# Kernel optimization log

Hardware: AMD Instinct MI355X
Metric: run time of the kernel (lower is better)

Reference implementation:

```python
import jax, jax.numpy as jnp
import numpy as np

N = 100000  # nodes
K = 6       # kNN neighbors (includes self, loop=True)


def _knn_edges(pos_np, k):
    """Exact kNN with self-loops, chunked to bound memory. Returns (src, dst) int32."""
    n = pos_np.shape[0]
    idx = np.empty((n, k), dtype=np.int32)
    sq = (pos_np ** 2).sum(1)
    cs = 512
    for s in range(0, n, cs):
        e = min(s + cs, n)
        d = sq[s:e, None] - 2.0 * (pos_np[s:e] @ pos_np.T) + sq[None, :]
        idx[s:e] = np.argpartition(d, k, axis=1)[:, :k].astype(np.int32)
    src = idx.reshape(-1)                                  # neighbors j
    dst = np.repeat(np.arange(n, dtype=np.int32), k)       # centers i
    return src, dst


def _linear_init(key, fan_in, fan_out):
    k1, k2 = jax.random.split(key)
    s = 1.0 / np.sqrt(fan_in)
    W = jax.random.uniform(k1, (fan_in, fan_out), minval=-s, maxval=s, dtype=jnp.float32)
    b = jax.random.uniform(k2, (fan_out,), minval=-s, maxval=s, dtype=jnp.float32)
    return W, b


def setup_inputs() -> dict:
    rng = np.random.default_rng(0)
    pos_np = rng.standard_normal((N, 3)).astype(np.float32)
    src, dst = _knn_edges(pos_np, K)
    edge_index = jnp.asarray(np.stack([src, dst]))

    key = jax.random.key(0)
    ks = jax.random.split(key, 6)
    W1a, b1a = _linear_init(ks[0], 3 + 3, 32)
    W1b, b1b = _linear_init(ks[1], 32, 32)
    W2a, b2a = _linear_init(ks[2], 32 + 3, 64)
    W2b, b2b = _linear_init(ks[3], 64, 64)
    W3a, b3a = _linear_init(ks[4], 64 + 3, 128)
    W3b, b3b = _linear_init(ks[5], 128, 128)

    return dict(pos=jnp.asarray(pos_np), edge_index=edge_index,
                W1a=W1a, b1a=b1a, W1b=W1b, b1b=b1b,
                W2a=W2a, b2a=b2a, W2b=W2b, b2b=b2b,
                W3a=W3a, b3a=b3a, W3b=W3b, b3b=b3b)


def _pointnet_conv(x, pos, src, dst, Wa, ba, Wb, bb):
    # message per edge (j->i): local_nn(concat(x_j, pos_j - pos_i)); max-aggregate at i
    m = jnp.concatenate([x[src], pos[src] - pos[dst]], axis=-1)  # [E, Cin+3]
    m = jax.nn.relu(m @ Wa + ba) @ Wb + bb                       # [E, Cout]
    return jax.ops.segment_max(m, dst, num_segments=N)           # [N, Cout]


def reference(pos, edge_index, W1a, b1a, W1b, b1b, W2a, b2a, W2b, b2b, W3a, b3a, W3b, b3b):
    src, dst = edge_index[0], edge_index[1]
    h = jax.nn.relu(_pointnet_conv(pos, pos, src, dst, W1a, b1a, W1b, b1b))
    h = jax.nn.relu(_pointnet_conv(h, pos, src, dst, W2a, b2a, W2b, b2b))
    h = jax.nn.relu(_pointnet_conv(h, pos, src, dst, W3a, b3a, W3b, b3b))
    return h
```

## Files before the change

### kernel.cpp

```cpp
#include <hip/hip_runtime.h>

#define NODES 100000
#define KNN 6

typedef unsigned short u16t;
typedef __attribute__((ext_vector_type(8))) short bf16x8;
typedef __attribute__((ext_vector_type(4))) float f32x4;
union U16 { uint4 u; bf16x8 b; };

__device__ inline f32x4 mfma16(bf16x8 a, bf16x8 b, f32x4 c) {
    return __builtin_amdgcn_mfma_f32_16x16x32_bf16(a, b, c, 0, 0, 0);
}
__device__ inline unsigned top2(unsigned u1, unsigned u0) {
    return __builtin_amdgcn_perm(u1, u0, 0x07060302u);
}
__device__ inline u16t bf16_rn(float x) {
    unsigned u = __float_as_uint(x);
    return (u16t)((u + 0x7FFF + ((u >> 16) & 1)) >> 16);
}
__device__ inline float bf16_f(u16t h) {
    return __uint_as_float(((unsigned)h) << 16);
}
__device__ inline void split_store(u16t* hp, u16t* lp, float v) {
    const unsigned u = __float_as_uint(v);
    *hp = (u16t)(u >> 16);
    const float hif = __uint_as_float(u & 0xFFFF0000u);
    *lp = (u16t)(__float_as_uint(v - hif) >> 16);
}

template <int CIN_, int N_>
__device__ void prep_dev(const float* __restrict__ W,
                         uint4* __restrict__ fh, uint4* __restrict__ fl, int idx) {
    constexpr int KT = (CIN_ + 31) / 32;
    constexpr int NTt = N_ / 16;
    if (idx >= NTt * KT * 64) return;
    const int lane = idx & 63;
    const int fk = idx >> 6;
    const int kt = fk % KT, t = fk / KT;
    const int n = t * 16 + (lane & 15);
    const int kbase = kt * 32 + (lane >> 4) * 8;
    unsigned h[4], l[4];
    for (int p = 0; p < 4; p++) {
        u16t hh[2], ll[2];
        for (int q = 0; q < 2; q++) {
            const int c = kbase + 2 * p + q;
            const float w = (c < CIN_) ? W[(size_t)c * N_ + n] : 0.f;
            const u16t hi = bf16_rn(w);
            hh[q] = hi;
            ll[q] = bf16_rn(w - bf16_f(hi));
        }
        h[p] = (unsigned)hh[0] | ((unsigned)hh[1] << 16);
        l[p] = (unsigned)ll[0] | ((unsigned)ll[1] << 16);
    }
    fh[idx] = make_uint4(h[0], h[1], h[2], h[3]);
    fl[idx] = make_uint4(l[0], l[1], l[2], l[3]);
}

__global__ void prep_all(const float* W1a, const float* W1b,
                         const float* W2a, const float* W2b,
                         const float* W3a, const float* W3b, uint4* wf) {
    const int b = blockIdx.x, t = threadIdx.x;
    if (b == 0)      prep_dev<6, 32>(W1a, wf + 0, wf + 128, t);
    else if (b == 1) prep_dev<32, 32>(W1b, wf + 256, wf + 384, t);
    else if (b < 4)  prep_dev<35, 64>(W2a, wf + 512, wf + 1024, (b - 2) * 256 + t);
    else if (b < 6)  prep_dev<64, 64>(W2b, wf + 1536, wf + 2048, (b - 4) * 256 + t);
    else if (b < 12) prep_dev<67, 128>(W3a, wf + 2560, wf + 4096, (b - 6) * 256 + t);
    else             prep_dev<128, 128>(W3b, wf + 5632, wf + 7680, (b - 12) * 256 + t);
}

template <int CX, int H, int NWAVE, int NB, bool OUTP>
__global__ __launch_bounds__(NWAVE * 64, 4) void pnconv_mfma(
    const u16t* __restrict__ xh, const u16t* __restrict__ xl,
    const float* __restrict__ pos, const int* __restrict__ ei,
    const uint4* __restrict__ wfa_hi, const uint4* __restrict__ wfa_lo,
    const float* __restrict__ ba,
    const uint4* __restrict__ wfb_hi, const uint4* __restrict__ wfb_lo,
    const float* __restrict__ bb,
    float* __restrict__ outf, u16t* __restrict__ oh, u16t* __restrict__ ol)
{
    constexpr int NTH = NWAVE * 64;
    constexpr int CIN = CX + 3;
    constexpr int K1T = (CIN + 31) / 32;
    constexpr int K2T = H / 32;
    constexpr int NW = (H / 16) / NWAVE;
    constexpr int E = NB * KNN;
    constexpr int MT1 = E / 16;
    constexpr int MT2 = E / 16;
    constexpr int K1P = K1T * 32 + 8;
    constexpr int K2P = K2T * 32 + 8;
    constexpr int APL = E * K1P;
    constexpr int HPL = E * K2P;
    constexpr int SM = (2 * APL > 2 * HPL) ? 2 * APL : 2 * HPL;
    static_assert(E % 48 == 0 && E <= NTH, "tile shape");
    static_assert(MT2 % 3 == 0, "slot perm needs m-triples");

    __shared__ __align__(16) u16t smem[SM];
    __shared__ int srcs[E];

    const int tid = threadIdx.x;
    const int lane = tid & 63, wv = tid >> 6;
    const int l15 = lane & 15, quad = lane >> 4;
    const int node0 = blockIdx.x * NB;
    const long e0 = (long)node0 * KNN;

    if (tid < E) srcs[tid] = ei[e0 + tid];

    U16 wah[2][NW], wal[2][NW];
#pragma unroll
    for (int t = 0; t < NW; t++) {
        const int fi = ((wv * NW + t) * K1T) * 64 + lane;
        wah[0][t].u = wfa_hi[fi];
        wal[0][t].u = wfa_lo[fi];
    }
    __syncthreads();

    if constexpr (CX % 8 == 0) {
        constexpr int C8 = CX / 8;
        for (int i = tid; i < E * C8; i += NTH) {
            const int e = i / C8, c0 = i % C8;
            const int c = (c0 + e) & (C8 - 1);
            const size_t sb = (size_t)srcs[e] * CX + c * 8;
            *(uint4*)&smem[e * K1P + c * 8] = *(const uint4*)&xh[sb];
            *(uint4*)&smem[APL + e * K1P + c * 8] = *(const uint4*)&xl[sb];
        }
    }
    for (int i = tid; i < E * 3; i += NTH) {
        const int e = i / 3, d = i - 3 * (i / 3);
        const int s = srcs[e], nd = node0 + e / KNN;
        const float sp = pos[3 * s + d];
        if constexpr (CX == 3)
            split_store(&smem[e * K1P + d], &smem[APL + e * K1P + d], sp);
        split_store(&smem[e * K1P + CX + d], &smem[APL + e * K1P + CX + d],
                    sp - pos[3 * nd + d]);
    }
    constexpr int PADA = (CIN + 7) & ~7;
    constexpr int NU4 = (K1P - PADA) / 8;
    for (int i = tid; i < 2 * E; i += NTH) {
        const int pl = (i >= E) ? 1 : 0;
        const int e = i - pl * E;
        u16t* row = &smem[pl * APL + e * K1P];
        for (int k = CIN; k < PADA; k++) row[k] = 0;
        for (int j = 0; j < NU4; j++) *(uint4*)&row[PADA + j * 8] = make_uint4(0, 0, 0, 0);
    }
    __syncthreads();

    f32x4 acc1[NW][MT1];
#pragma unroll
    for (int t = 0; t < NW; t++)
#pragma unroll
        for (int m = 0; m < MT1; m++) acc1[t][m] = (f32x4){0.f, 0.f, 0.f, 0.f};

#pragma unroll
    for (int kt = 0; kt < K1T; kt++) {
        const int cur = kt & 1, nxt = cur ^ 1;
        const int nkt = (kt + 1 < K1T) ? kt + 1 : kt;
#pragma unroll
        for (int t = 0; t < NW; t++) {
            const int fi = ((wv * NW + t) * K1T + nkt) * 64 + lane;
            wah[nxt][t].u = wfa_hi[fi];
            wal[nxt][t].u = wfa_lo[fi];
        }
#pragma unroll
        for (int m = 0; m < MT1; m++) {
            const u16t* p = &smem[(m * 16 + l15) * K1P + kt * 32 + quad * 8];
            U16 dh, dl;
            dh.u = *(const uint4*)p;
            dl.u = *(const uint4*)(p + APL);
#pragma unroll
            for (int t = 0; t < NW; t++) {
                acc1[t][m] = mfma16(wah[cur][t].b, dh.b, acc1[t][m]);
                acc1[t][m] = mfma16(wah[cur][t].b, dl.b, acc1[t][m]);
                acc1[t][m] = mfma16(wal[cur][t].b, dh.b, acc1[t][m]);
            }
        }
    }

    U16 wbh[2][NW], wbl[2][NW];
#pragma unroll
    for (int t = 0; t < NW; t++) {
        const int fi = ((wv * NW + t) * K2T) * 64 + lane;
        wbh[0][t].u = wfb_hi[fi];
        wbl[0][t].u = wfb_lo[fi];
    }
    __syncthreads();

#pragma unroll
    for (int t = 0; t < NW; t++) {
        const int khb = (wv * NW + t) * 16 + quad * 4;
        const float4 bs = *(const float4*)&ba[khb];
#pragma unroll
        for (int m = 0; m < MT1; m++) {
            const float v0 = fmaxf(acc1[t][m][0] + bs.x, 0.f);
            const float v1 = fmaxf(acc1[t][m][1] + bs.y, 0.f);
            const float v2 = fmaxf(acc1[t][m][2] + bs.z, 0.f);
            const float v3 = fmaxf(acc1[t][m][3] + bs.w, 0.f);
            const unsigned u0 = __float_as_uint(v0), u1 = __float_as_uint(v1);
            const unsigned u2 = __float_as_uint(v2), u3 = __float_as_uint(v3);
            uint2 hw, lw;
            hw.x = top2(u1, u0);
            hw.y = top2(u3, u2);
            const float l0 = v0 - __uint_as_float(u0 & 0xFFFF0000u);
            const float l1 = v1 - __uint_as_float(u1 & 0xFFFF0000u);
            const float l2 = v2 - __uint_as_float(u2 & 0xFFFF0000u);
            const float l3 = v3 - __uint_as_float(u3 & 0xFFFF0000u);
            lw.x = top2(__float_as_uint(l1), __float_as_uint(l0));
            lw.y = top2(__float_as_uint(l3), __float_as_uint(l2));
            u16t* wp = &smem[(m * 16 + l15) * K2P + khb];
            *(uint2*)wp = hw;
            *(uint2*)(wp + HPL) = lw;
        }
    }
    __syncthreads();

    int eaddr[MT2];
#pragma unroll
    for (int m = 0; m < MT2; m++) {
        const int nd_s = (m / 3) * 8 + 2 * (l15 >> 2) + ((l15 >> 1) & 1);
        const int i_s = (m % 3) * 2 + (l15 & 1);
        eaddr[m] = (nd_s * KNN + i_s) * K2P + quad * 8;
    }

    f32x4 acc2[NW][MT2];
#pragma unroll
    for (int t = 0; t < NW; t++)
#pragma unroll
        for (int m = 0; m < MT2; m++) acc2[t][m] = (f32x4){0.f, 0.f, 0.f, 0.f};

#pragma unroll
    for (int kt = 0; kt < K2T; kt++) {
        const int cur = kt & 1, nxt = cur ^ 1;
        const int nkt = (kt + 1 < K2T) ? kt + 1 : kt;
#pragma unroll
        for (int t = 0; t < NW; t++) {
            const int fi = ((wv * NW + t) * K2T + nkt) * 64 + lane;
            wbh[nxt][t].u = wfb_hi[fi];
            wbl[nxt][t].u = wfb_lo[fi];
        }
#pragma unroll
        for (int m = 0; m < MT2; m++) {
            const u16t* p = &smem[eaddr[m] + kt * 32];
            U16 dh, dl;
            dh.u = *(const uint4*)p;
            dl.u = *(const uint4*)(p + HPL);
#pragma unroll
            for (int t = 0; t < NW; t++) {
                acc2[t][m] = mfma16(dh.b, wbh[cur][t].b, acc2[t][m]);
                acc2[t][m] = mfma16(dh.b, wbl[cur][t].b, acc2[t][m]);
                acc2[t][m] = mfma16(dl.b, wbh[cur][t].b, acc2[t][m]);
            }
        }
    }

#pragma unroll
    for (int t = 0; t < NW; t++) {
        const int nb = (wv * NW + t) * 16;
        const float bias = bb[nb + l15];
#pragma unroll
        for (int g = 0; g < MT2 / 3; g++) {
#pragma unroll
            for (int rp = 0; rp < 2; rp++) {
                float v = fmaxf(
                    fmaxf(fmaxf(acc2[t][3 * g + 0][2 * rp], acc2[t][3 * g + 0][2 * rp + 1]),
                          fmaxf(acc2[t][3 * g + 1][2 * rp], acc2[t][3 * g + 1][2 * rp + 1])),
                    fmaxf(acc2[t][3 * g + 2][2 * rp], acc2[t][3 * g + 2][2 * rp + 1]));
                v = fmaxf(v + bias, 0.f);
                const int node = node0 + g * 8 + 2 * quad + rp;
                const size_t oidx = (size_t)node * H + nb + l15;
                if constexpr (OUTP) {
                    split_store(&oh[oidx], &ol[oidx], v);
                } else {
                    outf[oidx] = v;
                }
            }
        }
    }
}

extern "C" void kernel_launch(void* const* d_in, const int* in_sizes, int n_in,
                              void* d_out, int out_size, void* d_ws, size_t ws_size,
                              hipStream_t stream) {
    const float* pos = (const float*)d_in[0];
    const int* ei = (const int*)d_in[1];
    const float* W1a = (const float*)d_in[2];
    const float* b1a = (const float*)d_in[3];
    const float* W1b = (const float*)d_in[4];
    const float* b1b = (const float*)d_in[5];
    const float* W2a = (const float*)d_in[6];
    const float* b2a = (const float*)d_in[7];
    const float* W2b = (const float*)d_in[8];
    const float* b2b = (const float*)d_in[9];
    const float* W3a = (const float*)d_in[10];
    const float* b3a = (const float*)d_in[11];
    const float* W3b = (const float*)d_in[12];
    const float* b3b = (const float*)d_in[13];

    u16t* h1h = (u16t*)d_ws;
    u16t* h1l = h1h + (size_t)NODES * 32;
    u16t* h2h = h1l + (size_t)NODES * 32;
    u16t* h2l = h2h + (size_t)NODES * 64;
    uint4* wf = (uint4*)(h2l + (size_t)NODES * 64);

    prep_all<<<20, 256, 0, stream>>>(W1a, W1b, W2a, W2b, W3a, W3b, wf);

    pnconv_mfma<3, 32, 2, 16, true><<<NODES / 16, 128, 0, stream>>>(
        nullptr, nullptr, pos, ei,
        wf + 0, wf + 128, b1a, wf + 256, wf + 384, b1b,
        nullptr, h1h, h1l);

    pnconv_mfma<32, 64, 4, 16, true><<<NODES / 16, 256, 0, stream>>>(
        h1h, h1l, pos, ei,
        wf + 512, wf + 1024, b2a, wf + 1536, wf + 2048, b2b,
        nullptr, h2h, h2l);

    pnconv_mfma<64, 128, 4, 8, false><<<NODES / 8, 256, 0, stream>>>(
        h2h, h2l, pos, ei,
        wf + 2560, wf + 4096, b3a, wf + 5632, wf + 7680, b3b,
        (float*)d_out, nullptr, nullptr);
}
```

Measured before the change: 233.0 us.

## Load edge indices into registers and preload all weight fragments upfront

```diff
diff --git a/kernel.cpp b/kernel.cpp
--- a/kernel.cpp
+++ b/kernel.cpp
@@ -27,6 +27,7 @@
     const float hif = __uint_as_float(u & 0xFFFF0000u);
     *lp = (u16t)(__float_as_uint(v - hif) >> 16);
 }
+constexpr int cdiv(int a, int b) { return (a + b - 1) / b; }
 
 template <int CIN_, int N_>
 __device__ void prep_dev(const float* __restrict__ W,
@@ -69,7 +70,7 @@
 }
 
 template <int CX, int H, int NWAVE, int NB, bool OUTP>
-__global__ __launch_bounds__(NWAVE * 64, 4) void pnconv_mfma(
+__device__ __forceinline__ void pnconv_body(
     const u16t* __restrict__ xh, const u16t* __restrict__ xl,
     const float* __restrict__ pos, const int* __restrict__ ei,
     const uint4* __restrict__ wfa_hi, const uint4* __restrict__ wfa_lo,
@@ -91,11 +92,10 @@
     constexpr int APL = E * K1P;
     constexpr int HPL = E * K2P;
     constexpr int SM = (2 * APL > 2 * HPL) ? 2 * APL : 2 * HPL;
-    static_assert(E % 48 == 0 && E <= NTH, "tile shape");
+    static_assert(E % 48 == 0, "tile shape");
     static_assert(MT2 % 3 == 0, "slot perm needs m-triples");
 
     __shared__ __align__(16) u16t smem[SM];
-    __shared__ int srcs[E];
 
     const int tid = threadIdx.x;
     const int lane = tid & 63, wv = tid >> 6;
@@ -103,35 +103,58 @@
     const int node0 = blockIdx.x * NB;
     const long e0 = (long)node0 * KNN;
 
-    if (tid < E) srcs[tid] = ei[e0 + tid];
-
-    U16 wah[2][NW], wal[2][NW];
-#pragma unroll
-    for (int t = 0; t < NW; t++) {
-        const int fi = ((wv * NW + t) * K1T) * 64 + lane;
-        wah[0][t].u = wfa_hi[fi];
-        wal[0][t].u = wfa_lo[fi];
-    }
-    __syncthreads();
-
+    constexpr int C8 = (CX % 8 == 0) ? CX / 8 : 1;
+    constexpr int NGX = (CX % 8 == 0) ? cdiv(E * C8, NTH) : 1;
+    constexpr int NGP = cdiv(E * 3, NTH);
+    int sx_[NGX], sp_[NGP];
     if constexpr (CX % 8 == 0) {
-        constexpr int C8 = CX / 8;
-        for (int i = tid; i < E * C8; i += NTH) {
-            const int e = i / C8, c0 = i % C8;
-            const int c = (c0 + e) & (C8 - 1);
-            const size_t sb = (size_t)srcs[e] * CX + c * 8;
-            *(uint4*)&smem[e * K1P + c * 8] = *(const uint4*)&xh[sb];
-            *(uint4*)&smem[APL + e * K1P + c * 8] = *(const uint4*)&xl[sb];
-        }
-    }
-    for (int i = tid; i < E * 3; i += NTH) {
-        const int e = i / 3, d = i - 3 * (i / 3);
-        const int s = srcs[e], nd = node0 + e / KNN;
-        const float sp = pos[3 * s + d];
-        if constexpr (CX == 3)
-            split_store(&smem[e * K1P + d], &smem[APL + e * K1P + d], sp);
-        split_store(&smem[e * K1P + CX + d], &smem[APL + e * K1P + CX + d],
-                    sp - pos[3 * nd + d]);
+#pragma unroll
+        for (int k = 0; k < NGX; k++) {
+            const int i = tid + k * NTH;
+            sx_[k] = ei[e0 + ((i < E * C8) ? i / C8 : 0)];
+        }
+    }
+#pragma unroll
+    for (int k = 0; k < NGP; k++) {
+        const int i = tid + k * NTH;
+        sp_[k] = ei[e0 + ((i < E * 3) ? i / 3 : 0)];
+    }
+
+    U16 wah[NW][K1T], wal[NW][K1T];
+#pragma unroll
+    for (int t = 0; t < NW; t++)
+#pragma unroll
+        for (int kt = 0; kt < K1T; kt++) {
+            const int fi = ((wv * NW + t) * K1T + kt) * 64 + lane;
+            wah[t][kt].u = wfa_hi[fi];
+            wal[t][kt].u = wfa_lo[fi];
+        }
+
+    if constexpr (CX % 8 == 0) {
+#pragma unroll
+        for (int k = 0; k < NGX; k++) {
+            const int i = tid + k * NTH;
+            if (i < E * C8) {
+                const int e = i / C8, c0 = i % C8;
+                const int c = (c0 + e) & (C8 - 1);
+                const size_t sb = (size_t)sx_[k] * CX + c * 8;
+                *(uint4*)&smem[e * K1P + c * 8] = *(const uint4*)&xh[sb];
+                *(uint4*)&smem[APL + e * K1P + c * 8] = *(const uint4*)&xl[sb];
+            }
+        }
+    }
+#pragma unroll
+    for (int k = 0; k < NGP; k++) {
+        const int i = tid + k * NTH;
+        if (i < E * 3) {
+            const int e = i / 3, d = i - 3 * (i / 3);
+            const int s = sp_[k], nd = node0 + e / KNN;
+            const float sp = pos[3 * s + d];
+            if constexpr (CX == 3)
+                split_store(&smem[e * K1P + d], &smem[APL + e * K1P + d], sp);
+            split_store(&smem[e * K1P + CX + d], &smem[APL + e * K1P + CX + d],
+                        sp - pos[3 * nd + d]);
+        }
     }
     constexpr int PADA = (CIN + 7) & ~7;
     constexpr int NU4 = (K1P - PADA) / 8;
@@ -152,14 +175,6 @@
 
 #pragma unroll
     for (int kt = 0; kt < K1T; kt++) {
-        const int cur = kt & 1, nxt = cur ^ 1;
-        const int nkt = (kt + 1 < K1T) ? kt + 1 : kt;
-#pragma unroll
-        for (int t = 0; t < NW; t++) {
-            const int fi = ((wv * NW + t) * K1T + nkt) * 64 + lane;
-            wah[nxt][t].u = wfa_hi[fi];
-            wal[nxt][t].u = wfa_lo[fi];
-        }
 #pragma unroll
         for (int m = 0; m < MT1; m++) {
             const u16t* p = &smem[(m * 16 + l15) * K1P + kt * 32 + quad * 8];
@@ -168,20 +183,22 @@
             dl.u = *(const uint4*)(p + APL);
 #pragma unroll
             for (int t = 0; t < NW; t++) {
-                acc1[t][m] = mfma16(wah[cur][t].b, dh.b, acc1[t][m]);
-                acc1[t][m] = mfma16(wah[cur][t].b, dl.b, acc1[t][m]);
-                acc1[t][m] = mfma16(wal[cur][t].b, dh.b, acc1[t][m]);
+                acc1[t][m] = mfma16(wah[t][kt].b, dh.b, acc1[t][m]);
+                acc1[t][m] = mfma16(wah[t][kt].b, dl.b, acc1[t][m]);
+                acc1[t][m] = mfma16(wal[t][kt].b, dh.b, acc1[t][m]);
             }
         }
     }
 
-    U16 wbh[2][NW], wbl[2][NW];
-#pragma unroll
-    for (int t = 0; t < NW; t++) {
-        const int fi = ((wv * NW + t) * K2T) * 64 + lane;
-        wbh[0][t].u = wfb_hi[fi];
-        wbl[0][t].u = wfb_lo[fi];
-    }
+    U16 wbh[NW][K2T], wbl[NW][K2T];
+#pragma unroll
+    for (int t = 0; t < NW; t++)
+#pragma unroll
+        for (int kt = 0; kt < K2T; kt++) {
+            const int fi = ((wv * NW + t) * K2T + kt) * 64 + lane;
+            wbh[t][kt].u = wfb_hi[fi];
+            wbl[t][kt].u = wfb_lo[fi];
+        }
     __syncthreads();
 
 #pragma unroll
@@ -228,14 +245,6 @@
 
 #pragma unroll
     for (int kt = 0; kt < K2T; kt++) {
-        const int cur = kt & 1, nxt = cur ^ 1;
-        const int nkt = (kt + 1 < K2T) ? kt + 1 : kt;
-#pragma unroll
-        for (int t = 0; t < NW; t++) {
-            const int fi = ((wv * NW + t) * K2T + nkt) * 64 + lane;
-            wbh[nxt][t].u = wfb_hi[fi];
-            wbl[nxt][t].u = wfb_lo[fi];
-        }
 #pragma unroll
         for (int m = 0; m < MT2; m++) {
             const u16t* p = &smem[eaddr[m] + kt * 32];
@@ -244,9 +253,9 @@
             dl.u = *(const uint4*)(p + HPL);
 #pragma unroll
             for (int t = 0; t < NW; t++) {
-                acc2[t][m] = mfma16(dh.b, wbh[cur][t].b, acc2[t][m]);
-                acc2[t][m] = mfma16(dh.b, wbl[cur][t].b, acc2[t][m]);
-                acc2[t][m] = mfma16(dl.b, wbh[cur][t].b, acc2[t][m]);
+                acc2[t][m] = mfma16(dh.b, wbh[t][kt].b, acc2[t][m]);
+                acc2[t][m] = mfma16(dh.b, wbl[t][kt].b, acc2[t][m]);
+                acc2[t][m] = mfma16(dl.b, wbh[t][kt].b, acc2[t][m]);
             }
         }
     }
@@ -274,6 +283,30 @@
             }
         }
     }
+}
+
+__global__ __launch_bounds__(128, 4) void pn_l1(
+    const float* __restrict__ pos, const int* __restrict__ ei,
+    const uint4* __restrict__ wf, const float* __restrict__ b1a,
+    const float* __restrict__ b1b, u16t* __restrict__ oh, u16t* __restrict__ ol) {
+    pnconv_body<3, 32, 2, 16, true>(nullptr, nullptr, pos, ei,
+        wf + 0, wf + 128, b1a, wf + 256, wf + 384, b1b, nullptr, oh, ol);
+}
+__global__ __launch_bounds__(256, 4) void pn_l2(
+    const u16t* __restrict__ xh, const u16t* __restrict__ xl,
+    const float* __restrict__ pos, const int* __restrict__ ei,
+    const uint4* __restrict__ wf, const float* __restrict__ b2a,
+    const float* __restrict__ b2b, u16t* __restrict__ oh, u16t* __restrict__ ol) {
+    pnconv_body<32, 64, 4, 16, true>(xh, xl, pos, ei,
+        wf + 512, wf + 1024, b2a, wf + 1536, wf + 2048, b2b, nullptr, oh, ol);
+}
+__global__ __launch_bounds__(256, 4) void pn_l3(
+    const u16t* __restrict__ xh, const u16t* __restrict__ xl,
+    const float* __restrict__ pos, const int* __restrict__ ei,
+    const uint4* __restrict__ wf, const float* __restrict__ b3a,
+    const float* __restrict__ b3b, float* __restrict__ outf) {
+    pnconv_body<64, 128, 4, 8, false>(xh, xl, pos, ei,
+        wf + 2560, wf + 4096, b3a, wf + 5632, wf + 7680, b3b, outf, nullptr, nullptr);
 }
 
 extern "C" void kernel_launch(void* const* d_in, const int* in_sizes, int n_in,
@@ -301,19 +334,7 @@
     uint4* wf = (uint4*)(h2l + (size_t)NODES * 64);
 
     prep_all<<<20, 256, 0, stream>>>(W1a, W1b, W2a, W2b, W3a, W3b, wf);
-
-    pnconv_mfma<3, 32, 2, 16, true><<<NODES / 16, 128, 0, stream>>>(
-        nullptr, nullptr, pos, ei,
-        wf + 0, wf + 128, b1a, wf + 256, wf + 384, b1b,
-        nullptr, h1h, h1l);
-
-    pnconv_mfma<32, 64, 4, 16, true><<<NODES / 16, 256, 0, stream>>>(
-        h1h, h1l, pos, ei,
-        wf + 512, wf + 1024, b2a, wf + 1536, wf + 2048, b2b,
-        nullptr, h2h, h2l);
-
-    pnconv_mfma<64, 128, 4, 8, false><<<NODES / 8, 256, 0, stream>>>(
-        h2h, h2l, pos, ei,
-        wf + 2560, wf + 4096, b3a, wf + 5632, wf + 7680, b3b,
-        (float*)d_out, nullptr, nullptr);
-}
+    pn_l1<<<NODES / 16, 128, 0, stream>>>(pos, ei, wf, b1a, b1b, h1h, h1l);
+    pn_l2<<<NODES / 16, 256, 0, stream>>>(h1h, h1l, pos, ei, wf, b2a, b2b, h2h, h2l);
+    pn_l3<<<NODES / 8, 256, 0, stream>>>(h2h, h2l, pos, ei, wf, b3a, b3b, (float*)d_out);
+}
```

Measured after the change: 236.9 us. Within noise of the previous version (+1.7%).
